# Kernel tuning notes

Measured on AMD Instinct MI355X. Metric: run time of the kernel, lower is better.

The kernel has to match this reference:

```python
import jax, jax.numpy as jnp
import numpy as np

N, E, D = 50000, 800000, 128
BN_EPS = 1e-5


def setup_inputs() -> dict:
    key = jax.random.key(0)
    ks = jax.random.split(key, 6)
    x = jax.random.normal(ks[0], (N, D), dtype=jnp.float32)
    edge_index = jax.random.randint(ks[1], (2, E), 0, N, dtype=jnp.int32)
    edge_attr = jax.random.normal(ks[2], (E, D), dtype=jnp.float32)
    sc = 1.0 / np.sqrt(D).astype(np.float32)
    W1 = jax.random.normal(ks[3], (D, D), dtype=jnp.float32) * sc
    b1 = jnp.zeros((D,), jnp.float32)
    W2 = jax.random.normal(ks[4], (D, D), dtype=jnp.float32) * sc
    b2 = jnp.zeros((D,), jnp.float32)
    bn_w = jnp.ones((D,), jnp.float32)
    bn_b = jnp.zeros((D,), jnp.float32)
    return dict(x=x, edge_index=edge_index, edge_attr=edge_attr,
                W1=W1, b1=b1, W2=W2, b2=b2, bn_w=bn_w, bn_b=bn_b)


def reference(x, edge_index, edge_attr, W1, b1, W2, b2, bn_w, bn_b):
    # GINEConv: aggr_i = sum_{j->i} ReLU(x_j + e_ji); out = MLP((1+eps)*x + aggr), eps=0
    src, dst = edge_index[0], edge_index[1]
    msg = jax.nn.relu(x[src] + edge_attr)                     # [E, D] gather + elementwise
    aggr = jax.ops.segment_sum(msg, dst, num_segments=x.shape[0])  # scatter-add -> [N, D]
    h = x + aggr                                              # (1 + eps) * x, eps = 0
    h = jax.nn.relu(h @ W1 + b1) @ W2 + b2                    # GIN 2-layer MLP
    h = x + h                                                 # dropout(p=0) + residual
    # BatchNorm1d (training-mode batch statistics, biased variance)
    mean = jnp.mean(h, axis=0)
    var = jnp.var(h, axis=0)
    h = (h - mean) * jax.lax.rsqrt(var + BN_EPS) * bn_w + bn_b
    return h
```

## Files before the change

### kernel.cpp

```cpp
#include <hip/hip_runtime.h>
#include <stdint.h>

#define BN_EPS 1e-5f
#define WPAD 136

typedef short s8v __attribute__((ext_vector_type(8)));
typedef float f4v __attribute__((ext_vector_type(4)));

__device__ __forceinline__ float b2f(uint16_t h){
    uint32_t u = ((uint32_t)h) << 16; float f; __builtin_memcpy(&f, &u, 4); return f;
}
__device__ __forceinline__ uint16_t f2b(float f){
    uint32_t u; __builtin_memcpy(&u, &f, 4);
    uint32_t r = (u + 0x7fffu + ((u >> 16) & 1u)) >> 16;
    return (uint16_t)r;
}
__device__ __forceinline__ float lo16(uint32_t v){ return b2f((uint16_t)(v & 0xffffu)); }
__device__ __forceinline__ float hi16(uint32_t v){ return b2f((uint16_t)(v >> 16)); }
__device__ __forceinline__ uint32_t pack2(float a, float b){
    return (uint32_t)f2b(a) | ((uint32_t)f2b(b) << 16);
}

__global__ void k_detect(const uint32_t* __restrict__ xb, int* __restrict__ flag){
    int tid = threadIdx.x;
    uint32_t w = xb[tid];
    float v; __builtin_memcpy(&v, &w, 4);
    float a = fabsf(v);
    bool plaus = (v == 0.0f) || (a > 1e-6f && a < 1e6f);
    unsigned long long m = __ballot(plaus);
    if (tid == 0) flag[0] = (__popcll(m) >= 48) ? 1 : 0;
}

__global__ __launch_bounds__(256) void k_prep(const void* __restrict__ W1, const void* __restrict__ W2,
                                              const void* __restrict__ b1, const void* __restrict__ b2,
                                              const void* __restrict__ bnw, const void* __restrict__ bnb,
                                              const int* __restrict__ flag,
                                              uint16_t* __restrict__ WT1c, uint16_t* __restrict__ WT2c,
                                              float* __restrict__ vecs){
    bool f32 = flag[0] != 0;
    int i = blockIdx.x * 256 + threadIdx.x;
    if (i < 16384){
        int k = i >> 7, n = i & 127;
        float w1 = f32 ? ((const float*)W1)[i] : b2f(((const uint16_t*)W1)[i]);
        float w2 = f32 ? ((const float*)W2)[i] : b2f(((const uint16_t*)W2)[i]);
        WT1c[n * 128 + k] = f2b(w1);
        WT2c[n * 128 + k] = f2b(w2);
    }
    if (i < 128){
        vecs[i]       = f32 ? ((const float*)b1)[i]  : b2f(((const uint16_t*)b1)[i]);
        vecs[128 + i] = f32 ? ((const float*)b2)[i]  : b2f(((const uint16_t*)b2)[i]);
        vecs[256 + i] = f32 ? ((const float*)bnw)[i] : b2f(((const uint16_t*)bnw)[i]);
        vecs[384 + i] = f32 ? ((const float*)bnb)[i] : b2f(((const uint16_t*)bnb)[i]);
    }
}

__global__ void k_hist(const int* __restrict__ dst, int* __restrict__ counts, int N, int E){
    int e = blockIdx.x * 256 + threadIdx.x;
    if (e < E){
        int d = dst[e];
        if (d >= 0 && d < N) atomicAdd(&counts[d], 1);
    }
}

__global__ __launch_bounds__(1024) void k_scan(int* __restrict__ counts, int* __restrict__ cursor, int N){
    const int T = 1024;
    int tid = threadIdx.x;
    int chunk = (N + T - 1) / T;
    int beg = tid * chunk;
    int end = beg + chunk; if (end > N) end = N;
    int s = 0;
    for (int i = beg; i < end; ++i) s += counts[i];
    __shared__ int sm[T];
    sm[tid] = s; __syncthreads();
    for (int off = 1; off < T; off <<= 1){
        int v = (tid >= off) ? sm[tid - off] : 0;
        __syncthreads();
        sm[tid] += v;
        __syncthreads();
    }
    int run = sm[tid] - s;
    for (int i = beg; i < end; ++i){
        int c = counts[i];
        counts[i] = run; cursor[i] = run;
        run += c;
    }
    if (tid == T - 1){ counts[N] = run; cursor[N] = run; }
}

__global__ void k_scatter(const int* __restrict__ dst, const int* __restrict__ src,
                          int* __restrict__ cursor, int2* __restrict__ pe, int N, int E){
    int e = blockIdx.x * 256 + threadIdx.x;
    if (e < E){
        int d = dst[e];
        if (d >= 0 && d < N){
            int p = atomicAdd(&cursor[d], 1);
            if (p >= 0 && p < E){
                int2 v; v.x = e; v.y = src[e];
                pe[p] = v;
            }
        }
    }
}

__global__ __launch_bounds__(256) void k_agg(const void* __restrict__ x,
                                             const void* __restrict__ ea,
                                             const int2* __restrict__ pe,
                                             const int* __restrict__ offs,
                                             const int* __restrict__ flag,
                                             uint32_t* __restrict__ h0_2, int N, int E){
    int node = (blockIdx.x << 2) + (threadIdx.x >> 6);
    int lane = threadIdx.x & 63;
    if (node >= N) return;
    bool f32 = flag[0] != 0;
    int beg = offs[node], end = offs[node + 1];
    if (beg < 0) beg = 0;
    if (end > E) end = E;
    float a0 = 0.f, a1 = 0.f;

    const float2* xf = (const float2*)x;
    const float2* ef = (const float2*)ea;
    const uint32_t* xh = (const uint32_t*)x;
    const uint32_t* eh = (const uint32_t*)ea;

    for (int cb = beg; cb < end; cb += 64){
        int idx = cb + lane;
        int2 p;
        if (idx < end) p = pe[idx]; else { p.x = 0; p.y = 0; }
        int e = p.x, s = p.y;
        e = e < 0 ? 0 : (e >= E ? E - 1 : e);
        s = s < 0 ? 0 : (s >= N ? N - 1 : s);
        int m = end - cb; if (m > 64) m = 64;

        if (f32){
            int i = 0;
            for (; i + 4 <= m; i += 4){
                int e0 = __shfl(e, i),     s0 = __shfl(s, i);
                int e1 = __shfl(e, i + 1), s1 = __shfl(s, i + 1);
                int e2 = __shfl(e, i + 2), s2 = __shfl(s, i + 2);
                int e3 = __shfl(e, i + 3), s3 = __shfl(s, i + 3);
                float2 x0 = xf[(size_t)s0 * 64 + lane], v0 = ef[(size_t)e0 * 64 + lane];
                float2 x1 = xf[(size_t)s1 * 64 + lane], v1 = ef[(size_t)e1 * 64 + lane];
                float2 x2 = xf[(size_t)s2 * 64 + lane], v2 = ef[(size_t)e2 * 64 + lane];
                float2 x3 = xf[(size_t)s3 * 64 + lane], v3 = ef[(size_t)e3 * 64 + lane];
                a0 += fmaxf(x0.x + v0.x, 0.f); a1 += fmaxf(x0.y + v0.y, 0.f);
                a0 += fmaxf(x1.x + v1.x, 0.f); a1 += fmaxf(x1.y + v1.y, 0.f);
                a0 += fmaxf(x2.x + v2.x, 0.f); a1 += fmaxf(x2.y + v2.y, 0.f);
                a0 += fmaxf(x3.x + v3.x, 0.f); a1 += fmaxf(x3.y + v3.y, 0.f);
            }
            for (; i < m; ++i){
                int ei = __shfl(e, i), si = __shfl(s, i);
                float2 xv = xf[(size_t)si * 64 + lane];
                float2 ev = ef[(size_t)ei * 64 + lane];
                a0 += fmaxf(xv.x + ev.x, 0.f);
                a1 += fmaxf(xv.y + ev.y, 0.f);
            }
        } else {
            int i = 0;
            for (; i + 4 <= m; i += 4){
                int e0 = __shfl(e, i),     s0 = __shfl(s, i);
                int e1 = __shfl(e, i + 1), s1 = __shfl(s, i + 1);
                int e2 = __shfl(e, i + 2), s2 = __shfl(s, i + 2);
                int e3 = __shfl(e, i + 3), s3 = __shfl(s, i + 3);
                uint32_t x0 = xh[(size_t)s0 * 64 + lane], v0 = eh[(size_t)e0 * 64 + lane];
                uint32_t x1 = xh[(size_t)s1 * 64 + lane], v1 = eh[(size_t)e1 * 64 + lane];
                uint32_t x2 = xh[(size_t)s2 * 64 + lane], v2 = eh[(size_t)e2 * 64 + lane];
                uint32_t x3 = xh[(size_t)s3 * 64 + lane], v3 = eh[(size_t)e3 * 64 + lane];
                a0 += fmaxf(lo16(x0) + lo16(v0), 0.f); a1 += fmaxf(hi16(x0) + hi16(v0), 0.f);
                a0 += fmaxf(lo16(x1) + lo16(v1), 0.f); a1 += fmaxf(hi16(x1) + hi16(v1), 0.f);
                a0 += fmaxf(lo16(x2) + lo16(v2), 0.f); a1 += fmaxf(hi16(x2) + hi16(v2), 0.f);
                a0 += fmaxf(lo16(x3) + lo16(v3), 0.f); a1 += fmaxf(hi16(x3) + hi16(v3), 0.f);
            }
            for (; i < m; ++i){
                int ei = __shfl(e, i), si = __shfl(s, i);
                uint32_t xv = xh[(size_t)si * 64 + lane];
                uint32_t ev = eh[(size_t)ei * 64 + lane];
                a0 += fmaxf(lo16(xv) + lo16(ev), 0.f);
                a1 += fmaxf(hi16(xv) + hi16(ev), 0.f);
            }
        }
    }

    if (f32){
        float2 xn = xf[(size_t)node * 64 + lane];
        a0 += xn.x; a1 += xn.y;
    } else {
        uint32_t xn = xh[(size_t)node * 64 + lane];
        a0 += lo16(xn); a1 += hi16(xn);
    }
    h0_2[(size_t)node * 64 + lane] = pack2(a0, a1);
}

__global__ __launch_bounds__(256) void k_mlp(const uint16_t* __restrict__ h0,
                                             const uint16_t* __restrict__ WT1,
                                             const uint16_t* __restrict__ WT2,
                                             const float* __restrict__ vecs,
                                             const void* __restrict__ x,
                                             const int* __restrict__ flag,
                                             float* __restrict__ h3out,
                                             float* __restrict__ ssum,
                                             float* __restrict__ ssq, int N){
    __shared__ uint16_t Ws[128 * WPAD];
    __shared__ uint16_t H1[64 * WPAD];
    __shared__ float lsum[128], lsq[128];
    bool xf32 = flag[0] != 0;
    int tid = threadIdx.x;
    int lane = tid & 63;
    int w = tid >> 6;
    int r0 = blockIdx.x * 64;
    int mrow = lane & 15;
    int quad = lane >> 4;

    if (tid < 128){ lsum[tid] = 0.f; lsq[tid] = 0.f; }

    {
        const uint32_t* g = (const uint32_t*)WT1;
        #pragma unroll
        for (int j = 0; j < 32; ++j){
            int u = tid + 256 * j;
            int el = u << 1; int r = el >> 7, c = el & 127;
            *(uint32_t*)&Ws[r * WPAD + c] = g[u];
        }
    }
    __syncthreads();

    int arow = r0 + (w << 4) + mrow;
    int arow_c = arow < N ? arow : N - 1;
    s8v a[4];
    #pragma unroll
    for (int kt = 0; kt < 4; ++kt)
        a[kt] = *(const s8v*)(h0 + (size_t)arow_c * 128 + kt * 32 + quad * 8);

    #pragma unroll
    for (int nt = 0; nt < 8; ++nt){
        f4v acc = {0.f, 0.f, 0.f, 0.f};
        #pragma unroll
        for (int kt = 0; kt < 4; ++kt){
            s8v b = *(const s8v*)&Ws[(nt * 16 + mrow) * WPAD + kt * 32 + quad * 8];
            acc = __builtin_amdgcn_mfma_f32_16x16x32_bf16(a[kt], b, acc, 0, 0, 0);
        }
        int col = nt * 16 + mrow;
        float bias = vecs[col];
        #pragma unroll
        for (int r = 0; r < 4; ++r){
            float v = fmaxf(acc[r] + bias, 0.f);
            int lrow = (w << 4) + quad * 4 + r;
            H1[lrow * WPAD + col] = f2b(v);
        }
    }
    __syncthreads();

    {
        const uint32_t* g = (const uint32_t*)WT2;
        #pragma unroll
        for (int j = 0; j < 32; ++j){
            int u = tid + 256 * j;
            int el = u << 1; int r = el >> 7, c = el & 127;
            *(uint32_t*)&Ws[r * WPAD + c] = g[u];
        }
    }
    __syncthreads();

    s8v a2[4];
    #pragma unroll
    for (int kt = 0; kt < 4; ++kt)
        a2[kt] = *(const s8v*)&H1[((w << 4) + mrow) * WPAD + kt * 32 + quad * 8];

    const float* xf = (const float*)x;
    const uint16_t* xh = (const uint16_t*)x;

    #pragma unroll
    for (int nt = 0; nt < 8; ++nt){
        f4v acc = {0.f, 0.f, 0.f, 0.f};
        #pragma unroll
        for (int kt = 0; kt < 4; ++kt){
            s8v b = *(const s8v*)&Ws[(nt * 16 + mrow) * WPAD + kt * 32 + quad * 8];
            acc = __builtin_amdgcn_mfma_f32_16x16x32_bf16(a2[kt], b, acc, 0, 0, 0);
        }
        int col = nt * 16 + mrow;
        float bias = vecs[128 + col];
        float s_part = 0.f, q_part = 0.f;
        #pragma unroll
        for (int r = 0; r < 4; ++r){
            int grow = r0 + (w << 4) + quad * 4 + r;
            if (grow < N){
                float xv = xf32 ? xf[(size_t)grow * 128 + col]
                                : b2f(xh[(size_t)grow * 128 + col]);
                float h3 = xv + acc[r] + bias;
                h3out[(size_t)grow * 128 + col] = h3;
                s_part += h3; q_part += h3 * h3;
            }
        }
        float sr = s_part + __shfl_xor(s_part, 16);
        sr += __shfl_xor(sr, 32);
        float qr = q_part + __shfl_xor(q_part, 16);
        qr += __shfl_xor(qr, 32);
        if (quad == 0){
            atomicAdd(&lsum[col], sr);
            atomicAdd(&lsq[col], qr);
        }
    }
    __syncthreads();
    if (tid < 128){
        atomicAdd(&ssum[tid], lsum[tid]);
        atomicAdd(&ssq[tid], lsq[tid]);
    }
}

__global__ __launch_bounds__(256) void k_norm(void* __restrict__ out,
                                              const float2* __restrict__ h3,
                                              const int* __restrict__ flag,
                                              const float* __restrict__ ssum,
                                              const float* __restrict__ ssq,
                                              const float* __restrict__ vecs,
                                              int N, int total2){
    __shared__ float sc[128], sh[128];
    bool f32 = flag[0] != 0;
    int tid = threadIdx.x;
    if (tid < 128){
        float invN = 1.f / (float)N;
        float mean = ssum[tid] * invN;
        float var = ssq[tid] * invN - mean * mean;
        var = fmaxf(var, 0.f);
        float s = vecs[256 + tid] * rsqrtf(var + BN_EPS);
        sc[tid] = s;
        sh[tid] = vecs[384 + tid] - mean * s;
    }
    __syncthreads();
    for (int i = blockIdx.x * 256 + tid; i < total2; i += gridDim.x * 256){
        float2 h = h3[i];
        int cp = i & 63;
        float f0 = h.x * sc[2 * cp]     + sh[2 * cp];
        float f1 = h.y * sc[2 * cp + 1] + sh[2 * cp + 1];
        if (f32){ float2 o; o.x = f0; o.y = f1; ((float2*)out)[i] = o; }
        else    { ((uint32_t*)out)[i] = pack2(f0, f1); }
    }
}

extern "C" void kernel_launch(void* const* d_in, const int* in_sizes, int n_in,
                              void* d_out, int out_size, void* d_ws, size_t ws_size,
                              hipStream_t stream){
    const void* x   = d_in[0];
    const int*  ei  = (const int*)d_in[1];
    const void* ea  = d_in[2];
    const void* W1  = d_in[3];
    const void* b1  = d_in[4];
    const void* W2  = d_in[5];
    const void* b2  = d_in[6];
    const void* bnw = d_in[7];
    const void* bnb = d_in[8];

    int N = in_sizes[0] / 128;
    int E = in_sizes[1] / 2;
    const int* src = ei;
    const int* dst = ei + E;

    char* ws = (char*)d_ws;
    size_t off = 0;
    auto alloc = [&](size_t bytes){ size_t o = off; off += (bytes + 255) & ~(size_t)255; return o; };
    size_t o_counts = alloc((size_t)(N + 1) * 4);
    size_t o_cursor = alloc((size_t)(N + 1) * 4);
    size_t o_stats  = alloc(256 * 4);
    size_t o_flag   = alloc(4);
    size_t zeroBytes = off;
    size_t o_wt1  = alloc(16384 * 2);
    size_t o_wt2  = alloc(16384 * 2);
    size_t o_vecs = alloc(512 * 4);
    size_t o_h3   = alloc((size_t)N * 128 * 4);
    size_t o_pe   = alloc((size_t)E * 8);

    int E_used = E;
    if (off > ws_size){
        size_t fixed = o_pe;
        size_t avail = ws_size > fixed ? ws_size - fixed : 0;
        long long cap = (long long)(avail / 8);
        if (cap < E_used) E_used = (int)(cap < 0 ? 0 : cap);
    }

    int* counts = (int*)(ws + o_counts);
    int* cursor = (int*)(ws + o_cursor);
    float* ssum = (float*)(ws + o_stats);
    float* ssq  = ssum + 128;
    int* flag   = (int*)(ws + o_flag);
    uint16_t* WT1 = (uint16_t*)(ws + o_wt1);
    uint16_t* WT2 = (uint16_t*)(ws + o_wt2);
    float* vecs = (float*)(ws + o_vecs);
    float* h3   = (float*)(ws + o_h3);
    int2* pe    = (int2*)(ws + o_pe);
    uint16_t* h0 = (uint16_t*)d_out;

    hipMemsetAsync(d_ws, 0, zeroBytes, stream);

    k_detect<<<1, 64, 0, stream>>>((const uint32_t*)x, flag);
    k_hist<<<(E_used + 255) / 256, 256, 0, stream>>>(dst, counts, N, E_used);
    k_scan<<<1, 1024, 0, stream>>>(counts, cursor, N);
    k_scatter<<<(E_used + 255) / 256, 256, 0, stream>>>(dst, src, cursor, pe, N, E_used);
    k_prep<<<64, 256, 0, stream>>>(W1, W2, b1, b2, bnw, bnb, flag, WT1, WT2, vecs);
    k_agg<<<(N + 3) / 4, 256, 0, stream>>>(x, ea, pe, counts, flag,
                                           (uint32_t*)h0, N, E_used);
    k_mlp<<<(N + 63) / 64, 256, 0, stream>>>(h0, WT1, WT2, vecs, x, flag, h3, ssum, ssq, N);
    k_norm<<<2048, 256, 0, stream>>>(d_out, (const float2*)h3, flag, ssum, ssq,
                                     vecs, N, N * 64);
}
```

Measured before the change: 839.5 us.

## Fuse detect/prep into histogram launch and add nontemporal loads for streamed data

Removes the separate detect and prep kernels by merging weight prep into the histogram launch as extra blocks. Each kernel now recomputes the dtype flag per block from the first 64 words of x instead of reading a global flag. Nontemporal loads are added for dst/src indices, the permuted edge list and edge_attr in the gather, so single-use streams do not pollute cache. This cuts two launches but adds a small per-block detect plus barrier in agg, mlp and norm.

```diff
diff --git a/kernel.cpp b/kernel.cpp
--- a/kernel.cpp
+++ b/kernel.cpp
@@ -6,6 +6,7 @@
 
 typedef short s8v __attribute__((ext_vector_type(8)));
 typedef float f4v __attribute__((ext_vector_type(4)));
+typedef float f2v __attribute__((ext_vector_type(2)));
 
 __device__ __forceinline__ float b2f(uint16_t h){
     uint32_t u = ((uint32_t)h) << 16; float f; __builtin_memcpy(&f, &u, 4); return f;
@@ -21,44 +22,51 @@
     return (uint32_t)f2b(a) | ((uint32_t)f2b(b) << 16);
 }
 
-__global__ void k_detect(const uint32_t* __restrict__ xb, int* __restrict__ flag){
-    int tid = threadIdx.x;
-    uint32_t w = xb[tid];
-    float v; __builtin_memcpy(&v, &w, 4);
-    float a = fabsf(v);
-    bool plaus = (v == 0.0f) || (a > 1e-6f && a < 1e6f);
-    unsigned long long m = __ballot(plaus);
-    if (tid == 0) flag[0] = (__popcll(m) >= 48) ? 1 : 0;
-}
-
-__global__ __launch_bounds__(256) void k_prep(const void* __restrict__ W1, const void* __restrict__ W2,
-                                              const void* __restrict__ b1, const void* __restrict__ b2,
-                                              const void* __restrict__ bnw, const void* __restrict__ bnb,
-                                              const int* __restrict__ flag,
-                                              uint16_t* __restrict__ WT1c, uint16_t* __restrict__ WT2c,
-                                              float* __restrict__ vecs){
-    bool f32 = flag[0] != 0;
-    int i = blockIdx.x * 256 + threadIdx.x;
-    if (i < 16384){
-        int k = i >> 7, n = i & 127;
-        float w1 = f32 ? ((const float*)W1)[i] : b2f(((const uint16_t*)W1)[i]);
-        float w2 = f32 ? ((const float*)W2)[i] : b2f(((const uint16_t*)W2)[i]);
-        WT1c[n * 128 + k] = f2b(w1);
-        WT2c[n * 128 + k] = f2b(w2);
-    }
-    if (i < 128){
-        vecs[i]       = f32 ? ((const float*)b1)[i]  : b2f(((const uint16_t*)b1)[i]);
-        vecs[128 + i] = f32 ? ((const float*)b2)[i]  : b2f(((const uint16_t*)b2)[i]);
-        vecs[256 + i] = f32 ? ((const float*)bnw)[i] : b2f(((const uint16_t*)bnw)[i]);
-        vecs[384 + i] = f32 ? ((const float*)bnb)[i] : b2f(((const uint16_t*)bnb)[i]);
-    }
-}
-
-__global__ void k_hist(const int* __restrict__ dst, int* __restrict__ counts, int N, int E){
-    int e = blockIdx.x * 256 + threadIdx.x;
-    if (e < E){
-        int d = dst[e];
-        if (d >= 0 && d < N) atomicAdd(&counts[d], 1);
+__device__ __forceinline__ bool detect_f32_block(const uint32_t* __restrict__ xb, int tid, int* sflag){
+    if (tid < 64){
+        uint32_t w = xb[tid];
+        float v; __builtin_memcpy(&v, &w, 4);
+        float a = fabsf(v);
+        bool plaus = (v == 0.0f) || (a > 1e-6f && a < 1e6f);
+        unsigned long long m = __ballot(plaus);
+        if (tid == 0) *sflag = (__popcll(m) >= 48) ? 1 : 0;
+    }
+    __syncthreads();
+    return *sflag != 0;
+}
+
+__global__ __launch_bounds__(256) void k_hp(const int* __restrict__ dst,
+                                            int* __restrict__ counts, int N, int E, int histB,
+                                            const void* __restrict__ W1, const void* __restrict__ W2,
+                                            const void* __restrict__ b1, const void* __restrict__ b2,
+                                            const void* __restrict__ bnw, const void* __restrict__ bnb,
+                                            const void* __restrict__ x,
+                                            uint16_t* __restrict__ WT1c, uint16_t* __restrict__ WT2c,
+                                            float* __restrict__ vecs){
+    int bid = blockIdx.x;
+    if (bid < histB){
+        int e = bid * 256 + threadIdx.x;
+        if (e < E){
+            int d = __builtin_nontemporal_load(dst + e);
+            if (d >= 0 && d < N) atomicAdd(&counts[d], 1);
+        }
+    } else {
+        __shared__ int sflag;
+        bool f32 = detect_f32_block((const uint32_t*)x, threadIdx.x, &sflag);
+        int i = (bid - histB) * 256 + threadIdx.x;
+        if (i < 16384){
+            int k = i >> 7, n = i & 127;
+            float w1 = f32 ? ((const float*)W1)[i] : b2f(((const uint16_t*)W1)[i]);
+            float w2 = f32 ? ((const float*)W2)[i] : b2f(((const uint16_t*)W2)[i]);
+            WT1c[n * 128 + k] = f2b(w1);
+            WT2c[n * 128 + k] = f2b(w2);
+        }
+        if (i < 128){
+            vecs[i]       = f32 ? ((const float*)b1)[i]  : b2f(((const uint16_t*)b1)[i]);
+            vecs[128 + i] = f32 ? ((const float*)b2)[i]  : b2f(((const uint16_t*)b2)[i]);
+            vecs[256 + i] = f32 ? ((const float*)bnw)[i] : b2f(((const uint16_t*)bnw)[i]);
+            vecs[384 + i] = f32 ? ((const float*)bnb)[i] : b2f(((const uint16_t*)bnb)[i]);
+        }
     }
 }
 
@@ -91,11 +99,11 @@
                           int* __restrict__ cursor, int2* __restrict__ pe, int N, int E){
     int e = blockIdx.x * 256 + threadIdx.x;
     if (e < E){
-        int d = dst[e];
+        int d = __builtin_nontemporal_load(dst + e);
         if (d >= 0 && d < N){
             int p = atomicAdd(&cursor[d], 1);
             if (p >= 0 && p < E){
-                int2 v; v.x = e; v.y = src[e];
+                int2 v; v.x = e; v.y = __builtin_nontemporal_load(src + e);
                 pe[p] = v;
             }
         }
@@ -106,27 +114,28 @@
                                              const void* __restrict__ ea,
                                              const int2* __restrict__ pe,
                                              const int* __restrict__ offs,
-                                             const int* __restrict__ flag,
                                              uint32_t* __restrict__ h0_2, int N, int E){
+    __shared__ int sflag;
+    bool f32 = detect_f32_block((const uint32_t*)x, threadIdx.x, &sflag);
     int node = (blockIdx.x << 2) + (threadIdx.x >> 6);
     int lane = threadIdx.x & 63;
     if (node >= N) return;
-    bool f32 = flag[0] != 0;
     int beg = offs[node], end = offs[node + 1];
     if (beg < 0) beg = 0;
     if (end > E) end = E;
     float a0 = 0.f, a1 = 0.f;
 
-    const float2* xf = (const float2*)x;
-    const float2* ef = (const float2*)ea;
+    const f2v* xf = (const f2v*)x;
+    const f2v* ef = (const f2v*)ea;
     const uint32_t* xh = (const uint32_t*)x;
     const uint32_t* eh = (const uint32_t*)ea;
 
     for (int cb = beg; cb < end; cb += 64){
         int idx = cb + lane;
-        int2 p;
-        if (idx < end) p = pe[idx]; else { p.x = 0; p.y = 0; }
-        int e = p.x, s = p.y;
+        uint64_t pv = 0;
+        if (idx < end) pv = __builtin_nontemporal_load((const uint64_t*)pe + idx);
+        int e = (int)(uint32_t)(pv & 0xffffffffull);
+        int s = (int)(uint32_t)(pv >> 32);
         e = e < 0 ? 0 : (e >= E ? E - 1 : e);
         s = s < 0 ? 0 : (s >= N ? N - 1 : s);
         int m = end - cb; if (m > 64) m = 64;
@@ -138,10 +147,14 @@
                 int e1 = __shfl(e, i + 1), s1 = __shfl(s, i + 1);
                 int e2 = __shfl(e, i + 2), s2 = __shfl(s, i + 2);
                 int e3 = __shfl(e, i + 3), s3 = __shfl(s, i + 3);
-                float2 x0 = xf[(size_t)s0 * 64 + lane], v0 = ef[(size_t)e0 * 64 + lane];
-                float2 x1 = xf[(size_t)s1 * 64 + lane], v1 = ef[(size_t)e1 * 64 + lane];
-                float2 x2 = xf[(size_t)s2 * 64 + lane], v2 = ef[(size_t)e2 * 64 + lane];
-                float2 x3 = xf[(size_t)s3 * 64 + lane], v3 = ef[(size_t)e3 * 64 + lane];
+                f2v x0 = xf[(size_t)s0 * 64 + lane];
+                f2v x1 = xf[(size_t)s1 * 64 + lane];
+                f2v x2 = xf[(size_t)s2 * 64 + lane];
+                f2v x3 = xf[(size_t)s3 * 64 + lane];
+                f2v v0 = __builtin_nontemporal_load(ef + (size_t)e0 * 64 + lane);
+                f2v v1 = __builtin_nontemporal_load(ef + (size_t)e1 * 64 + lane);
+                f2v v2 = __builtin_nontemporal_load(ef + (size_t)e2 * 64 + lane);
+                f2v v3 = __builtin_nontemporal_load(ef + (size_t)e3 * 64 + lane);
                 a0 += fmaxf(x0.x + v0.x, 0.f); a1 += fmaxf(x0.y + v0.y, 0.f);
                 a0 += fmaxf(x1.x + v1.x, 0.f); a1 += fmaxf(x1.y + v1.y, 0.f);
                 a0 += fmaxf(x2.x + v2.x, 0.f); a1 += fmaxf(x2.y + v2.y, 0.f);
@@ -149,8 +162,8 @@
             }
             for (; i < m; ++i){
                 int ei = __shfl(e, i), si = __shfl(s, i);
-                float2 xv = xf[(size_t)si * 64 + lane];
-                float2 ev = ef[(size_t)ei * 64 + lane];
+                f2v xv = xf[(size_t)si * 64 + lane];
+                f2v ev = __builtin_nontemporal_load(ef + (size_t)ei * 64 + lane);
                 a0 += fmaxf(xv.x + ev.x, 0.f);
                 a1 += fmaxf(xv.y + ev.y, 0.f);
             }
@@ -161,10 +174,14 @@
                 int e1 = __shfl(e, i + 1), s1 = __shfl(s, i + 1);
                 int e2 = __shfl(e, i + 2), s2 = __shfl(s, i + 2);
                 int e3 = __shfl(e, i + 3), s3 = __shfl(s, i + 3);
-                uint32_t x0 = xh[(size_t)s0 * 64 + lane], v0 = eh[(size_t)e0 * 64 + lane];
-                uint32_t x1 = xh[(size_t)s1 * 64 + lane], v1 = eh[(size_t)e1 * 64 + lane];
-                uint32_t x2 = xh[(size_t)s2 * 64 + lane], v2 = eh[(size_t)e2 * 64 + lane];
-                uint32_t x3 = xh[(size_t)s3 * 64 + lane], v3 = eh[(size_t)e3 * 64 + lane];
+                uint32_t x0 = xh[(size_t)s0 * 64 + lane];
+                uint32_t x1 = xh[(size_t)s1 * 64 + lane];
+                uint32_t x2 = xh[(size_t)s2 * 64 + lane];
+                uint32_t x3 = xh[(size_t)s3 * 64 + lane];
+                uint32_t v0 = __builtin_nontemporal_load(eh + (size_t)e0 * 64 + lane);
+                uint32_t v1 = __builtin_nontemporal_load(eh + (size_t)e1 * 64 + lane);
+                uint32_t v2 = __builtin_nontemporal_load(eh + (size_t)e2 * 64 + lane);
+                uint32_t v3 = __builtin_nontemporal_load(eh + (size_t)e3 * 64 + lane);
                 a0 += fmaxf(lo16(x0) + lo16(v0), 0.f); a1 += fmaxf(hi16(x0) + hi16(v0), 0.f);
                 a0 += fmaxf(lo16(x1) + lo16(v1), 0.f); a1 += fmaxf(hi16(x1) + hi16(v1), 0.f);
                 a0 += fmaxf(lo16(x2) + lo16(v2), 0.f); a1 += fmaxf(hi16(x2) + hi16(v2), 0.f);
@@ -173,7 +190,7 @@
             for (; i < m; ++i){
                 int ei = __shfl(e, i), si = __shfl(s, i);
                 uint32_t xv = xh[(size_t)si * 64 + lane];
-                uint32_t ev = eh[(size_t)ei * 64 + lane];
+                uint32_t ev = __builtin_nontemporal_load(eh + (size_t)ei * 64 + lane);
                 a0 += fmaxf(lo16(xv) + lo16(ev), 0.f);
                 a1 += fmaxf(hi16(xv) + hi16(ev), 0.f);
             }
@@ -181,7 +198,7 @@
     }
 
     if (f32){
-        float2 xn = xf[(size_t)node * 64 + lane];
+        f2v xn = xf[(size_t)node * 64 + lane];
         a0 += xn.x; a1 += xn.y;
     } else {
         uint32_t xn = xh[(size_t)node * 64 + lane];
@@ -195,15 +212,15 @@
                                              const uint16_t* __restrict__ WT2,
                                              const float* __restrict__ vecs,
                                              const void* __restrict__ x,
-                                             const int* __restrict__ flag,
                                              float* __restrict__ h3out,
                                              float* __restrict__ ssum,
                                              float* __restrict__ ssq, int N){
     __shared__ uint16_t Ws[128 * WPAD];
     __shared__ uint16_t H1[64 * WPAD];
     __shared__ float lsum[128], lsq[128];
-    bool xf32 = flag[0] != 0;
+    __shared__ int sflag;
     int tid = threadIdx.x;
+    bool xf32 = detect_f32_block((const uint32_t*)x, tid, &sflag);
     int lane = tid & 63;
     int w = tid >> 6;
     int r0 = blockIdx.x * 64;
@@ -308,14 +325,15 @@
 
 __global__ __launch_bounds__(256) void k_norm(void* __restrict__ out,
                                               const float2* __restrict__ h3,
-                                              const int* __restrict__ flag,
+                                              const void* __restrict__ x,
                                               const float* __restrict__ ssum,
                                               const float* __restrict__ ssq,
                                               const float* __restrict__ vecs,
                                               int N, int total2){
     __shared__ float sc[128], sh[128];
-    bool f32 = flag[0] != 0;
+    __shared__ int sflag;
     int tid = threadIdx.x;
+    bool f32 = detect_f32_block((const uint32_t*)x, tid, &sflag);
     if (tid < 128){
         float invN = 1.f / (float)N;
         float mean = ssum[tid] * invN;
@@ -360,7 +378,6 @@
     size_t o_counts = alloc((size_t)(N + 1) * 4);
     size_t o_cursor = alloc((size_t)(N + 1) * 4);
     size_t o_stats  = alloc(256 * 4);
-    size_t o_flag   = alloc(4);
     size_t zeroBytes = off;
     size_t o_wt1  = alloc(16384 * 2);
     size_t o_wt2  = alloc(16384 * 2);
@@ -380,7 +397,6 @@
     int* cursor = (int*)(ws + o_cursor);
     float* ssum = (float*)(ws + o_stats);
     float* ssq  = ssum + 128;
-    int* flag   = (int*)(ws + o_flag);
     uint16_t* WT1 = (uint16_t*)(ws + o_wt1);
     uint16_t* WT2 = (uint16_t*)(ws + o_wt2);
     float* vecs = (float*)(ws + o_vecs);
@@ -390,14 +406,13 @@
 
     hipMemsetAsync(d_ws, 0, zeroBytes, stream);
 
-    k_detect<<<1, 64, 0, stream>>>((const uint32_t*)x, flag);
-    k_hist<<<(E_used + 255) / 256, 256, 0, stream>>>(dst, counts, N, E_used);
+    int histB = (E_used + 255) / 256;
+    k_hp<<<histB + 64, 256, 0, stream>>>(dst, counts, N, E_used, histB,
+                                         W1, W2, b1, b2, bnw, bnb, x, WT1, WT2, vecs);
     k_scan<<<1, 1024, 0, stream>>>(counts, cursor, N);
     k_scatter<<<(E_used + 255) / 256, 256, 0, stream>>>(dst, src, cursor, pe, N, E_used);
-    k_prep<<<64, 256, 0, stream>>>(W1, W2, b1, b2, bnw, bnb, flag, WT1, WT2, vecs);
-    k_agg<<<(N + 3) / 4, 256, 0, stream>>>(x, ea, pe, counts, flag,
-                                           (uint32_t*)h0, N, E_used);
-    k_mlp<<<(N + 63) / 64, 256, 0, stream>>>(h0, WT1, WT2, vecs, x, flag, h3, ssum, ssq, N);
-    k_norm<<<2048, 256, 0, stream>>>(d_out, (const float2*)h3, flag, ssum, ssq,
+    k_agg<<<(N + 3) / 4, 256, 0, stream>>>(x, ea, pe, counts, (uint32_t*)h0, N, E_used);
+    k_mlp<<<(N + 63) / 64, 256, 0, stream>>>(h0, WT1, WT2, vecs, x, h3, ssum, ssq, N);
+    k_norm<<<2048, 256, 0, stream>>>(d_out, (const float2*)h3, x, ssum, ssq,
                                      vecs, N, N * 64);
 }
```

Measured after the change: 823.8 us. About the same (-1.9%).
